# Performance work log

Hardware: AMD Instinct MI355X
Metric: run time of the kernel (lower is better)

Reference implementation:

```python
import jax, jax.numpy as jnp
import numpy as np

H = 2048          # hidden_size
NQ = 16           # num_q_heads
NKV = 4           # num_kv_heads
HD = H // NQ      # head_dim = 128
REP = NQ // NKV   # kv repeat factor
FF = 8192         # intermediate_size
B, S = 2, 2048
EPS = 1e-6


def setup_inputs() -> dict:
    key = jax.random.key(0)
    ks = jax.random.split(key, 12)
    sd = 0.02
    return {
        "hidden_states": jax.random.normal(ks[0], (B, S, H), jnp.float32),
        "Wq": jax.random.normal(ks[1], (H, H), jnp.float32) * sd,
        "bq": jnp.zeros((H,), jnp.float32),
        "Wk": jax.random.normal(ks[2], (H, NKV * HD), jnp.float32) * sd,
        "bk": jnp.zeros((NKV * HD,), jnp.float32),
        "Wv": jax.random.normal(ks[3], (H, NKV * HD), jnp.float32) * sd,
        "bv": jnp.zeros((NKV * HD,), jnp.float32),
        "Wo": jax.random.normal(ks[4], (H, H), jnp.float32) * sd,
        "bo": jnp.zeros((H,), jnp.float32),
        "W1": jax.random.normal(ks[5], (H, FF), jnp.float32) * sd,
        "b1": jnp.zeros((FF,), jnp.float32),
        "W2": jax.random.normal(ks[6], (FF, H), jnp.float32) * sd,
        "b2": jnp.zeros((H,), jnp.float32),
        "g1": jnp.ones((H,), jnp.float32),  # ln1 weight
        "g2": jnp.ones((H,), jnp.float32),  # ln2 weight
    }


def _rmsnorm(x, g):
    rms = jnp.sqrt(jnp.mean(x * x, axis=-1, keepdims=True) + EPS)
    return g * (x / rms)


def _attention(x, Wq, bq, Wk, bk, Wv, bv, Wo, bo):
    b, s, _ = x.shape
    q = (x @ Wq + bq).reshape(b, s, NQ, HD).transpose(0, 2, 1, 3)    # [b,hq,s,d]
    k = (x @ Wk + bk).reshape(b, s, NKV, HD).transpose(0, 2, 1, 3)   # [b,hkv,s,d]
    v = (x @ Wv + bv).reshape(b, s, NKV, HD).transpose(0, 2, 1, 3)
    k = jnp.repeat(k, REP, axis=1)  # GQA: repeat_interleave over head dim
    v = jnp.repeat(v, REP, axis=1)
    scale = 1.0 / np.sqrt(HD).astype(np.float32)
    scores = jnp.einsum("bhqd,bhkd->bhqk", q, k) * scale
    causal = jnp.triu(jnp.ones((s, s), bool), k=1)                   # True above diag
    scores = jnp.where(causal[None, None], -jnp.inf, scores)
    probs = jax.nn.softmax(scores, axis=-1)
    ctx = jnp.einsum("bhqk,bhkd->bhqd", probs, v)
    ctx = ctx.transpose(0, 2, 1, 3).reshape(b, s, H)
    return ctx @ Wo + bo


def reference(hidden_states, Wq, bq, Wk, bk, Wv, bv, Wo, bo, W1, b1, W2, b2, g1, g2):
    x = hidden_states
    # pre-norm attention block
    x = x + _attention(_rmsnorm(x, g1), Wq, bq, Wk, bk, Wv, bv, Wo, bo)
    # pre-norm FFN block (exact GELU, matching torch nn.GELU default)
    h = _rmsnorm(x, g2)
    h = jax.nn.gelu(h @ W1 + b1, approximate=False) @ W2 + b2
    return x + h
```

## Files before the change

### kernel.cpp

```cpp
#include <hip/hip_runtime.h>
#include <cstdint>

#define H_    2048
#define NQ_   16
#define NKV_  4
#define HD_   128
#define FF_   8192
#define B_    2
#define S_    2048
#define TOK   (B_*S_)
#define QKVN  (H_ + 2*NKV_*HD_)
#define KVB   64

typedef __bf16 bf16;
typedef bf16  bf16x8 __attribute__((ext_vector_type(8)));
typedef float f32x4  __attribute__((ext_vector_type(4)));

typedef __attribute__((address_space(1))) void as1_void;
typedef __attribute__((address_space(3))) void as3_void;

__device__ __forceinline__ void gload_lds16(const void* g, void* l) {
    __builtin_amdgcn_global_load_lds((as1_void*)g, (as3_void*)l, 16, 0, 0);
}

__global__ __launch_bounds__(256) void wtrans_kernel(
    const float* __restrict__ W, bf16* __restrict__ Wt, int K, int N, int outOff)
{
    __shared__ float tile[32][33];
    const int n0 = (int)blockIdx.x * 32;
    const int k0 = (int)blockIdx.y * 32;
    const int c  = (int)threadIdx.x & 31;
    const int r  = (int)threadIdx.x >> 5;
#pragma unroll
    for (int i = 0; i < 4; ++i)
        tile[r + i*8][c] = W[(size_t)(k0 + r + i*8) * N + n0 + c];
    __syncthreads();
#pragma unroll
    for (int i = 0; i < 4; ++i)
        Wt[(size_t)(outOff + n0 + r + i*8) * K + k0 + c] = (bf16)tile[c][r + i*8];
}

__global__ void biaspack_kernel(const float* __restrict__ bq, const float* __restrict__ bk,
                                const float* __restrict__ bv, float* __restrict__ out)
{
    const int i = (int)(blockIdx.x * 256 + threadIdx.x);
    out[i] = (i < H_) ? bq[i] : (i < H_ + NKV_*HD_ ? bk[i - H_] : bv[i - H_ - NKV_*HD_]);
}

__global__ __launch_bounds__(256) void rmsnorm_kernel(
    const float* __restrict__ x, const float* __restrict__ g, bf16* __restrict__ y)
{
    const int row = (int)blockIdx.x;
    const int tid = (int)threadIdx.x;
    const float* xr = x + (size_t)row * H_;
    const float4 a = *(const float4*)(xr + tid*8);
    const float4 c = *(const float4*)(xr + tid*8 + 4);
    float ss = a.x*a.x + a.y*a.y + a.z*a.z + a.w*a.w
             + c.x*c.x + c.y*c.y + c.z*c.z + c.w*c.w;
#pragma unroll
    for (int d = 1; d < 64; d <<= 1) ss += __shfl_xor(ss, d);
    __shared__ float red[4];
    if ((tid & 63) == 0) red[tid >> 6] = ss;
    __syncthreads();
    const float inv = rsqrtf((red[0]+red[1]+red[2]+red[3]) * (1.0f/H_) + 1e-6f);
    const float vals[8] = {a.x,a.y,a.z,a.w,c.x,c.y,c.z,c.w};
    const float* gp = g + tid*8;
    bf16x8 outv;
#pragma unroll
    for (int e = 0; e < 8; ++e) outv[e] = (bf16)(vals[e] * inv * gp[e]);
    *(bf16x8*)(y + (size_t)row * H_ + tid*8) = outv;
}

__global__ __launch_bounds__(256) void vtrans_kernel(
    const bf16* __restrict__ qkv, bf16* __restrict__ Vt)
{
    __shared__ bf16 tile[32][33];
    const int tt = (int)blockIdx.x;
    const int d0 = (int)blockIdx.y * 32;
    const int kh = (int)blockIdx.z;
    const int b  = (tt*32) / S_;
    const int s0 = (tt*32) % S_;
    const int c = (int)threadIdx.x & 31;
    const int r = (int)threadIdx.x >> 5;
#pragma unroll
    for (int i = 0; i < 4; ++i)
        tile[r + i*8][c] = qkv[(size_t)(tt*32 + r + i*8)*QKVN + H_ + NKV_*HD_ + kh*HD_ + d0 + c];
    __syncthreads();
#pragma unroll
    for (int i = 0; i < 4; ++i)
        Vt[((size_t)(b*NKV_ + kh)*HD_ + d0 + r + i*8)*S_ + s0 + c] = tile[c][r + i*8];
}

template<int MODE>
__global__ __launch_bounds__(256) void gemm_kernel(
    const bf16* __restrict__ A, const bf16* __restrict__ Bt,
    const float* __restrict__ bias, const float* __restrict__ resid,
    void* __restrict__ Cout, int M, int N, int K)
{
    __shared__ bf16 lA[128*64];
    __shared__ bf16 lB[128*64];
    const int tid  = (int)threadIdx.x;
    const int wid  = tid >> 6;
    const int lane = tid & 63;
    const int lr   = lane & 15;
    const int lg   = lane >> 4;
    const int m0 = (int)blockIdx.y * 128;
    const int n0 = (int)blockIdx.x * 128;
    const int wm = (wid >> 1) * 64;
    const int wn = (wid & 1) * 64;

    f32x4 acc[4][4] = {};

    const int sRow = wid*32 + (lane >> 3);
    const int sCol = ((lane & 7) ^ (lane >> 3)) * 8;
    const bf16* aSrc = A  + (size_t)(m0 + sRow) * K + sCol;
    const bf16* bSrc = Bt + (size_t)(n0 + sRow) * K + sCol;

    for (int k0 = 0; k0 < K; k0 += 64) {
#pragma unroll
        for (int i = 0; i < 4; ++i) {
            gload_lds16(aSrc + (size_t)(i*8)*K + k0, &lA[(wid*32 + i*8)*64]);
            gload_lds16(bSrc + (size_t)(i*8)*K + k0, &lB[(wid*32 + i*8)*64]);
        }
        __syncthreads();
#pragma unroll
        for (int kk = 0; kk < 64; kk += 32) {
            const int ks = (kk + lg*8) ^ ((lr & 7) * 8);
            bf16x8 af[4], bfr[4];
#pragma unroll
            for (int i = 0; i < 4; ++i)
                af[i] = *(const bf16x8*)&lA[(wm + i*16 + lr)*64 + ks];
#pragma unroll
            for (int j = 0; j < 4; ++j)
                bfr[j] = *(const bf16x8*)&lB[(wn + j*16 + lr)*64 + ks];
#pragma unroll
            for (int i = 0; i < 4; ++i)
#pragma unroll
                for (int j = 0; j < 4; ++j)
                    acc[i][j] = __builtin_amdgcn_mfma_f32_16x16x32_bf16(
                        af[i], bfr[j], acc[i][j], 0, 0, 0);
        }
        __syncthreads();
    }

#pragma unroll
    for (int j = 0; j < 4; ++j) {
        const int col = n0 + wn + j*16 + lr;
        const float bj = bias[col];
#pragma unroll
        for (int i = 0; i < 4; ++i) {
            const int row0 = m0 + wm + i*16 + lg*4;
#pragma unroll
            for (int rr = 0; rr < 4; ++rr) {
                float v = acc[i][j][rr] + bj;
                const size_t idx = (size_t)(row0 + rr) * N + col;
                if (MODE == 2) {
                    ((float*)Cout)[idx] = v + resid[idx];
                } else {
                    if (MODE == 1) v = 0.5f * v * (1.0f + erff(v * 0.70710678118654752f));
                    ((bf16*)Cout)[idx] = (bf16)v;
                }
            }
        }
    }
}

__global__ __launch_bounds__(256) void attn_kernel(
    const bf16* __restrict__ qkv, const bf16* __restrict__ Vt,
    bf16* __restrict__ ctx)
{
    __shared__ bf16 lK[2][KVB*HD_];
    __shared__ bf16 lV[2][HD_*KVB];
    __shared__ bf16 lP[4][16*72];
    const int tid  = (int)threadIdx.x;
    const int wid  = tid >> 6;
    const int lane = tid & 63;
    const int lr   = lane & 15;
    const int lg   = lane >> 4;
    const int qt = (int)gridDim.x - 1 - (int)blockIdx.x;
    const int h = (int)blockIdx.y, b = (int)blockIdx.z;
    const int kh = h >> 2;
    const int qb = qt * 64;
    const int qw = qb + wid * 16;
    const float scale = 0.08838834764831845f;

    const bf16* kB[4];
    const bf16* vB[4];
#pragma unroll
    for (int i = 0; i < 4; ++i) {
        const int kRow = (wid*4 + i)*4 + (lane >> 4);
        const int kCol = ((lane & 15) ^ (kRow & 7)) * 8;
        kB[i] = qkv + (size_t)(b*S_ + kRow)*QKVN + H_ + kh*HD_ + kCol;
        const int vRow = (wid*4 + i)*8 + (lane >> 3);
        const int vCol = ((lane & 7) ^ (vRow & 7)) * 8;
        vB[i] = Vt + ((size_t)(b*NKV_ + kh)*HD_ + vRow)*S_ + vCol;
    }

    bf16x8 qf[4];
    {
        const bf16* qp = qkv + (size_t)(b*S_ + qw + lr)*QKVN + h*HD_ + lg*8;
#pragma unroll
        for (int t = 0; t < 4; ++t) qf[t] = *(const bf16x8*)(qp + t*32);
    }

    f32x4 o[8] = {};
    float mrow[4] = {-__builtin_inff(), -__builtin_inff(), -__builtin_inff(), -__builtin_inff()};
    float lrow[4] = {0.f, 0.f, 0.f, 0.f};
    const int nt = qt + 1;

#pragma unroll
    for (int i = 0; i < 4; ++i) {
        gload_lds16(kB[i], &lK[0][(wid*4 + i)*4*HD_]);
        gload_lds16(vB[i], &lV[0][(wid*4 + i)*8*KVB]);
    }

    int cur = 0;
    for (int t = 0; t < nt; ++t) {
        __syncthreads();
        if (t + 1 < nt) {
            const size_t kAdd = (size_t)(t+1)*KVB*QKVN;
            const size_t vAdd = (size_t)(t+1)*KVB;
#pragma unroll
            for (int i = 0; i < 4; ++i) {
                gload_lds16(kB[i] + kAdd, &lK[cur^1][(wid*4 + i)*4*HD_]);
                gload_lds16(vB[i] + vAdd, &lV[cur^1][(wid*4 + i)*8*KVB]);
            }
        }
        const int kv0 = t * KVB;

        f32x4 s[4] = {};
#pragma unroll
        for (int sub = 0; sub < 4; ++sub) {
            const int krow = sub*16 + lr;
            const bf16* kr = &lK[cur][krow*HD_];
            const int sw = (krow & 7) * 8;
#pragma unroll
            for (int d = 0; d < 4; ++d) {
                const bf16x8 kf = *(const bf16x8*)(kr + ((d*32 + lg*8) ^ sw));
                s[sub] = __builtin_amdgcn_mfma_f32_16x16x32_bf16(qf[d], kf, s[sub], 0, 0, 0);
            }
        }

        float p[4][4], rmax[4];
        if (t == qt) {
#pragma unroll
            for (int rr = 0; rr < 4; ++rr) {
                const int q = qw + lg*4 + rr;
                rmax[rr] = -__builtin_inff();
#pragma unroll
                for (int sub = 0; sub < 4; ++sub) {
                    const int kv = kv0 + sub*16 + lr;
                    const float v = s[sub][rr] * scale;
                    p[sub][rr] = (kv <= q) ? v : -__builtin_inff();
                    rmax[rr] = fmaxf(rmax[rr], p[sub][rr]);
                }
            }
        } else {
#pragma unroll
            for (int rr = 0; rr < 4; ++rr) {
                rmax[rr] = -__builtin_inff();
#pragma unroll
                for (int sub = 0; sub < 4; ++sub) {
                    p[sub][rr] = s[sub][rr] * scale;
                    rmax[rr] = fmaxf(rmax[rr], p[sub][rr]);
                }
            }
        }
#pragma unroll
        for (int d = 1; d < 16; d <<= 1)
#pragma unroll
            for (int rr = 0; rr < 4; ++rr)
                rmax[rr] = fmaxf(rmax[rr], __shfl_xor(rmax[rr], d));

        float fsc[4], rsum[4];
#pragma unroll
        for (int rr = 0; rr < 4; ++rr) {
            const float mn = fmaxf(mrow[rr], rmax[rr]);
            fsc[rr]  = __expf(mrow[rr] - mn);
            mrow[rr] = mn;
            rsum[rr] = 0.f;
#pragma unroll
            for (int sub = 0; sub < 4; ++sub) {
                p[sub][rr] = __expf(p[sub][rr] - mn);
                rsum[rr] += p[sub][rr];
            }
        }
#pragma unroll
        for (int d = 1; d < 16; d <<= 1)
#pragma unroll
            for (int rr = 0; rr < 4; ++rr)
                rsum[rr] += __shfl_xor(rsum[rr], d);
#pragma unroll
        for (int rr = 0; rr < 4; ++rr) lrow[rr] = lrow[rr]*fsc[rr] + rsum[rr];
#pragma unroll
        for (int dch = 0; dch < 8; ++dch)
#pragma unroll
            for (int rr = 0; rr < 4; ++rr) o[dch][rr] *= fsc[rr];

#pragma unroll
        for (int sub = 0; sub < 4; ++sub)
#pragma unroll
            for (int rr = 0; rr < 4; ++rr)
                lP[wid][(lg*4 + rr)*72 + sub*16 + lr] = (bf16)p[sub][rr];
        bf16x8 pf[2];
#pragma unroll
        for (int kk = 0; kk < 2; ++kk)
            pf[kk] = *(const bf16x8*)&lP[wid][lr*72 + kk*32 + lg*8];

#pragma unroll
        for (int dch = 0; dch < 8; ++dch) {
            const bf16* vr = &lV[cur][(dch*16 + lr)*KVB];
            const int sw = (lr & 7) * 8;
#pragma unroll
            for (int kk = 0; kk < 2; ++kk) {
                const bf16x8 vf = *(const bf16x8*)(vr + ((kk*32 + lg*8) ^ sw));
                o[dch] = __builtin_amdgcn_mfma_f32_16x16x32_bf16(pf[kk], vf, o[dch], 0, 0, 0);
            }
        }
        cur ^= 1;
    }

#pragma unroll
    for (int rr = 0; rr < 4; ++rr) {
        const float inv = 1.0f / lrow[rr];
        bf16* cp = ctx + (size_t)(b*S_ + qw + lg*4 + rr) * H_ + h*HD_ + lr;
#pragma unroll
        for (int dch = 0; dch < 8; ++dch)
            cp[dch*16] = (bf16)(o[dch][rr] * inv);
    }
}

extern "C" void kernel_launch(void* const* d_in, const int* in_sizes, int n_in,
                              void* d_out, int out_size, void* d_ws, size_t ws_size,
                              hipStream_t stream)
{
    const float* hidden = (const float*)d_in[0];
    const float* Wq = (const float*)d_in[1];
    const float* bq = (const float*)d_in[2];
    const float* Wk = (const float*)d_in[3];
    const float* bk = (const float*)d_in[4];
    const float* Wv = (const float*)d_in[5];
    const float* bv = (const float*)d_in[6];
    const float* Wo = (const float*)d_in[7];
    const float* bo = (const float*)d_in[8];
    const float* W1 = (const float*)d_in[9];
    const float* b1 = (const float*)d_in[10];
    const float* W2 = (const float*)d_in[11];
    const float* b2 = (const float*)d_in[12];
    const float* g1 = (const float*)d_in[13];
    const float* g2 = (const float*)d_in[14];
    float* out = (float*)d_out;

    char* p = (char*)d_ws;
    auto alloc = [&](size_t bytes) { char* r = p; p += (bytes + 255) & ~(size_t)255; return r; };
    bf16*  wt_qkv = (bf16*)alloc((size_t)QKVN * H_ * 2);
    bf16*  wo_t   = (bf16*)alloc((size_t)H_ * H_ * 2);
    bf16*  w1_t   = (bf16*)alloc((size_t)FF_ * H_ * 2);
    bf16*  w2_t   = (bf16*)alloc((size_t)H_ * FF_ * 2);
    float* bqkv   = (float*)alloc((size_t)QKVN * 4);
    bf16*  xn1    = (bf16*)alloc((size_t)TOK * H_ * 2);
    bf16*  qkv    = (bf16*)alloc((size_t)TOK * QKVN * 2);
    bf16*  ctxb   = (bf16*)alloc((size_t)TOK * H_ * 2);
    float* x1     = (float*)alloc((size_t)TOK * H_ * 4);
    bf16*  xn2    = (bf16*)alloc((size_t)TOK * H_ * 2);
    bf16*  ffn    = (bf16*)alloc((size_t)TOK * FF_ * 2);
    bf16*  vt     = xn1;

    const dim3 blk(256);
    biaspack_kernel<<<dim3(QKVN/256), blk, 0, stream>>>(bq, bk, bv, bqkv);
    wtrans_kernel<<<dim3(H_/32,  H_/32),  blk, 0, stream>>>(Wq, wt_qkv, H_, H_,  0);
    wtrans_kernel<<<dim3(512/32, H_/32),  blk, 0, stream>>>(Wk, wt_qkv, H_, 512, H_);
    wtrans_kernel<<<dim3(512/32, H_/32),  blk, 0, stream>>>(Wv, wt_qkv, H_, 512, H_ + 512);
    wtrans_kernel<<<dim3(H_/32,  H_/32),  blk, 0, stream>>>(Wo, wo_t,   H_, H_,  0);
    wtrans_kernel<<<dim3(FF_/32, H_/32),  blk, 0, stream>>>(W1, w1_t,   H_, FF_, 0);
    wtrans_kernel<<<dim3(H_/32,  FF_/32), blk, 0, stream>>>(W2, w2_t,   FF_, H_, 0);

    rmsnorm_kernel<<<dim3(TOK), blk, 0, stream>>>(hidden, g1, xn1);
    gemm_kernel<0><<<dim3(QKVN/128, TOK/128), blk, 0, stream>>>(
        xn1, wt_qkv, bqkv, nullptr, qkv, TOK, QKVN, H_);
    vtrans_kernel<<<dim3(TOK/32, HD_/32, NKV_), blk, 0, stream>>>(qkv, vt);
    attn_kernel<<<dim3(S_/64, NQ_, B_), blk, 0, stream>>>(qkv, vt, ctxb);
    gemm_kernel<2><<<dim3(H_/128, TOK/128), blk, 0, stream>>>(
        ctxb, wo_t, bo, hidden, x1, TOK, H_, H_);
    rmsnorm_kernel<<<dim3(TOK), blk, 0, stream>>>(x1, g2, xn2);
    gemm_kernel<1><<<dim3(FF_/128, TOK/128), blk, 0, stream>>>(
        xn2, w1_t, b1, nullptr, ffn, TOK, FF_, H_);
    gemm_kernel<2><<<dim3(H_/128, TOK/128), blk, 0, stream>>>(
        ffn, w2_t, b2, x1, out, TOK, H_, FF_);
}
```

Measured before the change: 758.1 us.

## Replace GEMM with 256x128 triple-buffered 8-wave pipelined kernel

The old 128x128 single-buffered GEMM is replaced by a 512-thread kernel with 256x128 tiles and a three-stage LDS ring. Global-to-LDS prefetch of tile t+2 is interleaved with MFMA work in two half-phases, and s_setprio, sched_barrier and explicit waitcnts are used to overlap memory with compute. It also remaps workgroup IDs in an XCD-aware order to improve L2 locality, and uses a different LDS swizzle. The aim is to hide load latency and raise MFMA utilisation in the GEMMs that dominate runtime. The cost is more LDS per block, one block per CU, and fragile hand-managed vmcnt accounting.

Result: no change. 753.1 us (-0.7%).

```diff
diff --git a/kernel.cpp b/kernel.cpp
--- a/kernel.cpp
+++ b/kernel.cpp
@@ -12,6 +12,10 @@
 #define QKVN  (H_ + 2*NKV_*HD_)
 #define KVB   64
 
+#define BM 256
+#define BN 128
+#define BKG 64
+
 typedef __bf16 bf16;
 typedef bf16  bf16x8 __attribute__((ext_vector_type(8)));
 typedef float f32x4  __attribute__((ext_vector_type(4)));
@@ -92,67 +96,136 @@
 }
 
 template<int MODE>
-__global__ __launch_bounds__(256) void gemm_kernel(
+__global__ __launch_bounds__(512, 1) void gemm2_kernel(
     const bf16* __restrict__ A, const bf16* __restrict__ Bt,
     const float* __restrict__ bias, const float* __restrict__ resid,
     void* __restrict__ Cout, int M, int N, int K)
 {
-    __shared__ bf16 lA[128*64];
-    __shared__ bf16 lB[128*64];
+    __shared__ bf16 lA[3][BM*BKG];
+    __shared__ bf16 lB[3][BN*BKG];
     const int tid  = (int)threadIdx.x;
     const int wid  = tid >> 6;
     const int lane = tid & 63;
     const int lr   = lane & 15;
     const int lg   = lane >> 4;
-    const int m0 = (int)blockIdx.y * 128;
-    const int n0 = (int)blockIdx.x * 128;
-    const int wm = (wid >> 1) * 64;
-    const int wn = (wid & 1) * 64;
+
+    const int gx  = (int)gridDim.x;
+    const int nwg = gx * (int)gridDim.y;
+    int wg = (int)blockIdx.y * gx + (int)blockIdx.x;
+    if ((nwg & 7) == 0) wg = (wg & 7) * (nwg >> 3) + (wg >> 3);
+    const int n0 = (wg % gx) * BN;
+    const int m0 = (wg / gx) * BM;
+
+    const int wr = wid >> 1;
+    const int wc = wid & 1;
+
+    const int srow = wid*8 + (lane >> 3);
+    const int scol = ((lane & 7) * 8) ^ ((wid & 1) * 16);
+    const bf16* aS = A  + (size_t)(m0 + srow) * K + scol;
+    const bf16* bS = Bt + (size_t)(n0 + srow) * K + scol;
 
     f32x4 acc[4][4] = {};
-
-    const int sRow = wid*32 + (lane >> 3);
-    const int sCol = ((lane & 7) ^ (lane >> 3)) * 8;
-    const bf16* aSrc = A  + (size_t)(m0 + sRow) * K + sCol;
-    const bf16* bSrc = Bt + (size_t)(n0 + sRow) * K + sCol;
-
-    for (int k0 = 0; k0 < K; k0 += 64) {
-#pragma unroll
-        for (int i = 0; i < 4; ++i) {
-            gload_lds16(aSrc + (size_t)(i*8)*K + k0, &lA[(wid*32 + i*8)*64]);
-            gload_lds16(bSrc + (size_t)(i*8)*K + k0, &lB[(wid*32 + i*8)*64]);
-        }
-        __syncthreads();
-#pragma unroll
-        for (int kk = 0; kk < 64; kk += 32) {
-            const int ks = (kk + lg*8) ^ ((lr & 7) * 8);
-            bf16x8 af[4], bfr[4];
-#pragma unroll
-            for (int i = 0; i < 4; ++i)
-                af[i] = *(const bf16x8*)&lA[(wm + i*16 + lr)*64 + ks];
-#pragma unroll
-            for (int j = 0; j < 4; ++j)
-                bfr[j] = *(const bf16x8*)&lB[(wn + j*16 + lr)*64 + ks];
-#pragma unroll
-            for (int i = 0; i < 4; ++i)
-#pragma unroll
-                for (int j = 0; j < 4; ++j)
-                    acc[i][j] = __builtin_amdgcn_mfma_f32_16x16x32_bf16(
-                        af[i], bfr[j], acc[i][j], 0, 0, 0);
-        }
-        __syncthreads();
-    }
-
-#pragma unroll
-    for (int j = 0; j < 4; ++j) {
-        const int col = n0 + wn + j*16 + lr;
+    const int nt = K / BKG;
+
+#pragma unroll
+    for (int i = 0; i < 4; ++i)
+        gload_lds16(aS + (size_t)i*64*K, &lA[0][(i*64 + wid*8)*BKG]);
+#pragma unroll
+    for (int j = 0; j < 2; ++j)
+        gload_lds16(bS + (size_t)j*64*K, &lB[0][(j*64 + wid*8)*BKG]);
+#pragma unroll
+    for (int i = 0; i < 4; ++i)
+        gload_lds16(aS + (size_t)i*64*K + BKG, &lA[1][(i*64 + wid*8)*BKG]);
+#pragma unroll
+    for (int j = 0; j < 2; ++j)
+        gload_lds16(bS + (size_t)j*64*K + BKG, &lB[1][(j*64 + wid*8)*BKG]);
+    asm volatile("s_waitcnt vmcnt(6)" ::: "memory");
+    __builtin_amdgcn_s_barrier();
+
+    const int sw = ((lane >> 3) & 1) * 16;
+    int cur = 0;
+    for (int t = 0; t < nt; ++t) {
+        const bf16* lAc = lA[cur];
+        const bf16* lBc = lB[cur];
+        const int   pc  = (cur + 2 >= 3) ? cur - 1 : cur + 2;
+        const size_t nk0 = (size_t)(t + 2) * BKG;
+        const bool  pf  = (t + 2) < nt;
+
+        bf16x8 af[2][2], bfr[4][2];
+#pragma unroll
+        for (int mf = 0; mf < 2; ++mf)
+#pragma unroll
+            for (int ks = 0; ks < 2; ++ks)
+                af[mf][ks] = *(const bf16x8*)&lAc[(wr*64 + mf*16 + lr)*BKG + ((ks*32 + lg*8) ^ sw)];
+#pragma unroll
+        for (int nf = 0; nf < 4; ++nf)
+#pragma unroll
+            for (int ks = 0; ks < 2; ++ks)
+                bfr[nf][ks] = *(const bf16x8*)&lBc[(wc*64 + nf*16 + lr)*BKG + ((ks*32 + lg*8) ^ sw)];
+        if (pf) {
+            gload_lds16(aS + (size_t)0*64*K + nk0, &lA[pc][(0*64 + wid*8)*BKG]);
+            gload_lds16(aS + (size_t)1*64*K + nk0, &lA[pc][(1*64 + wid*8)*BKG]);
+            gload_lds16(aS + (size_t)2*64*K + nk0, &lA[pc][(2*64 + wid*8)*BKG]);
+        }
+        __builtin_amdgcn_s_barrier();
+        asm volatile("s_waitcnt lgkmcnt(0)" ::: "memory");
+        __builtin_amdgcn_sched_barrier(0);
+        __builtin_amdgcn_s_setprio(1);
+#pragma unroll
+        for (int ks = 0; ks < 2; ++ks)
+#pragma unroll
+            for (int mf = 0; mf < 2; ++mf)
+#pragma unroll
+                for (int nf = 0; nf < 4; ++nf)
+                    acc[mf][nf] = __builtin_amdgcn_mfma_f32_16x16x32_bf16(
+                        af[mf][ks], bfr[nf][ks], acc[mf][nf], 0, 0, 0);
+        __builtin_amdgcn_s_setprio(0);
+        __builtin_amdgcn_sched_barrier(0);
+        __builtin_amdgcn_s_barrier();
+
+        bf16x8 af2[2][2];
+#pragma unroll
+        for (int mf = 0; mf < 2; ++mf)
+#pragma unroll
+            for (int ks = 0; ks < 2; ++ks)
+                af2[mf][ks] = *(const bf16x8*)&lAc[(wr*64 + (mf+2)*16 + lr)*BKG + ((ks*32 + lg*8) ^ sw)];
+        if (pf) {
+            gload_lds16(aS + (size_t)3*64*K + nk0, &lA[pc][(3*64 + wid*8)*BKG]);
+            gload_lds16(bS + (size_t)0*64*K + nk0, &lB[pc][(0*64 + wid*8)*BKG]);
+            gload_lds16(bS + (size_t)1*64*K + nk0, &lB[pc][(1*64 + wid*8)*BKG]);
+            asm volatile("s_waitcnt vmcnt(6)" ::: "memory");
+        } else {
+            asm volatile("s_waitcnt vmcnt(0)" ::: "memory");
+        }
+        __builtin_amdgcn_s_barrier();
+        asm volatile("s_waitcnt lgkmcnt(0)" ::: "memory");
+        __builtin_amdgcn_sched_barrier(0);
+        __builtin_amdgcn_s_setprio(1);
+#pragma unroll
+        for (int ks = 0; ks < 2; ++ks)
+#pragma unroll
+            for (int mf = 0; mf < 2; ++mf)
+#pragma unroll
+                for (int nf = 0; nf < 4; ++nf)
+                    acc[mf+2][nf] = __builtin_amdgcn_mfma_f32_16x16x32_bf16(
+                        af2[mf][ks], bfr[nf][ks], acc[mf+2][nf], 0, 0, 0);
+        __builtin_amdgcn_s_setprio(0);
+        __builtin_amdgcn_sched_barrier(0);
+        __builtin_amdgcn_s_barrier();
+
+        cur = (cur + 1 >= 3) ? 0 : cur + 1;
+    }
+
+#pragma unroll
+    for (int nf = 0; nf < 4; ++nf) {
+        const int col = n0 + wc*64 + nf*16 + lr;
         const float bj = bias[col];
 #pragma unroll
-        for (int i = 0; i < 4; ++i) {
-            const int row0 = m0 + wm + i*16 + lg*4;
+        for (int mf = 0; mf < 4; ++mf) {
+            const int row0 = m0 + wr*64 + mf*16 + lg*4;
 #pragma unroll
             for (int rr = 0; rr < 4; ++rr) {
-                float v = acc[i][j][rr] + bj;
+                float v = acc[mf][nf][rr] + bj;
                 const size_t idx = (size_t)(row0 + rr) * N + col;
                 if (MODE == 2) {
                     ((float*)Cout)[idx] = v + resid[idx];
@@ -233,10 +306,10 @@
         for (int sub = 0; sub < 4; ++sub) {
             const int krow = sub*16 + lr;
             const bf16* kr = &lK[cur][krow*HD_];
-            const int sw = (krow & 7) * 8;
+            const int swk = (krow & 7) * 8;
 #pragma unroll
             for (int d = 0; d < 4; ++d) {
-                const bf16x8 kf = *(const bf16x8*)(kr + ((d*32 + lg*8) ^ sw));
+                const bf16x8 kf = *(const bf16x8*)(kr + ((d*32 + lg*8) ^ swk));
                 s[sub] = __builtin_amdgcn_mfma_f32_16x16x32_bf16(qf[d], kf, s[sub], 0, 0, 0);
             }
         }
@@ -302,19 +375,19 @@
 #pragma unroll
             for (int rr = 0; rr < 4; ++rr)
                 lP[wid][(lg*4 + rr)*72 + sub*16 + lr] = (bf16)p[sub][rr];
-        bf16x8 pf[2];
+        bf16x8 pfr[2];
 #pragma unroll
         for (int kk = 0; kk < 2; ++kk)
-            pf[kk] = *(const bf16x8*)&lP[wid][lr*72 + kk*32 + lg*8];
+            pfr[kk] = *(const bf16x8*)&lP[wid][lr*72 + kk*32 + lg*8];
 
 #pragma unroll
         for (int dch = 0; dch < 8; ++dch) {
             const bf16* vr = &lV[cur][(dch*16 + lr)*KVB];
-            const int sw = (lr & 7) * 8;
+            const int swv = (lr & 7) * 8;
 #pragma unroll
             for (int kk = 0; kk < 2; ++kk) {
-                const bf16x8 vf = *(const bf16x8*)(vr + ((kk*32 + lg*8) ^ sw));
-                o[dch] = __builtin_amdgcn_mfma_f32_16x16x32_bf16(pf[kk], vf, o[dch], 0, 0, 0);
+                const bf16x8 vf = *(const bf16x8*)(vr + ((kk*32 + lg*8) ^ swv));
+                o[dch] = __builtin_amdgcn_mfma_f32_16x16x32_bf16(pfr[kk], vf, o[dch], 0, 0, 0);
             }
         }
         cur ^= 1;
@@ -367,6 +440,7 @@
     bf16*  vt     = xn1;
 
     const dim3 blk(256);
+    const dim3 blk2(512);
     biaspack_kernel<<<dim3(QKVN/256), blk, 0, stream>>>(bq, bk, bv, bqkv);
     wtrans_kernel<<<dim3(H_/32,  H_/32),  blk, 0, stream>>>(Wq, wt_qkv, H_, H_,  0);
     wtrans_kernel<<<dim3(512/32, H_/32),  blk, 0, stream>>>(Wk, wt_qkv, H_, 512, H_);
@@ -376,15 +450,15 @@
     wtrans_kernel<<<dim3(H_/32,  FF_/32), blk, 0, stream>>>(W2, w2_t,   FF_, H_, 0);
 
     rmsnorm_kernel<<<dim3(TOK), blk, 0, stream>>>(hidden, g1, xn1);
-    gemm_kernel<0><<<dim3(QKVN/128, TOK/128), blk, 0, stream>>>(
+    gemm2_kernel<0><<<dim3(QKVN/BN, TOK/BM), blk2, 0, stream>>>(
         xn1, wt_qkv, bqkv, nullptr, qkv, TOK, QKVN, H_);
     vtrans_kernel<<<dim3(TOK/32, HD_/32, NKV_), blk, 0, stream>>>(qkv, vt);
     attn_kernel<<<dim3(S_/64, NQ_, B_), blk, 0, stream>>>(qkv, vt, ctxb);
-    gemm_kernel<2><<<dim3(H_/128, TOK/128), blk, 0, stream>>>(
+    gemm2_kernel<2><<<dim3(H_/BN, TOK/BM), blk2, 0, stream>>>(
         ctxb, wo_t, bo, hidden, x1, TOK, H_, H_);
     rmsnorm_kernel<<<dim3(TOK), blk, 0, stream>>>(x1, g2, xn2);
-    gemm_kernel<1><<<dim3(FF_/128, TOK/128), blk, 0, stream>>>(
+    gemm2_kernel<1><<<dim3(FF_/BN, TOK/BM), blk2, 0, stream>>>(
         xn2, w1_t, b1, nullptr, ffn, TOK, FF_, H_);
-    gemm_kernel<2><<<dim3(H_/128, TOK/128), blk, 0, stream>>>(
+    gemm2_kernel<2><<<dim3(H_/BN, TOK/BM), blk2, 0, stream>>>(
         ffn, w2_t, b2, x1, out, TOK, H_, FF_);
 }
```

## Replace GEMM with 256x256 double-buffered 8-wave kernel and split-K W2 GEMM

Applied to the files above, without the earlier changes.

Swaps the 128x128 single-buffered GEMM for a 256x256 tile kernel with 512 threads. It double-buffers LDS through async global-to-LDS loads and interleaves MFMA clusters with staged loads under explicit waitcnt and barriers. Workgroup IDs are remapped for locality, and setprio is raised during MFMA bursts. The FFN down-projection (K=8192) now uses split-K over two partitions that write bf16 partials into the freed W1 buffer, followed by a reduce kernel that adds bias and residual. The aim is higher MFMA utilisation and better tile reuse. The cost is bf16 rounding of the partial sums, an extra reduce pass, and heavy LDS use (128KB per block).

New measurement: 757.4 us. Within noise of the previous version (-0.1%).

```diff
diff --git a/kernel.cpp b/kernel.cpp
--- a/kernel.cpp
+++ b/kernel.cpp
@@ -92,70 +92,177 @@
 }
 
 template<int MODE>
-__global__ __launch_bounds__(256) void gemm_kernel(
+__global__ __launch_bounds__(512, 2) void gemm3_kernel(
     const bf16* __restrict__ A, const bf16* __restrict__ Bt,
     const float* __restrict__ bias, const float* __restrict__ resid,
-    void* __restrict__ Cout, int M, int N, int K)
-{
-    __shared__ bf16 lA[128*64];
-    __shared__ bf16 lB[128*64];
+    void* __restrict__ Cout, int M, int N, int Kf, int Ks)
+{
+    __shared__ bf16 lA[2][256*64];
+    __shared__ bf16 lB[2][256*64];
     const int tid  = (int)threadIdx.x;
     const int wid  = tid >> 6;
     const int lane = tid & 63;
     const int lr   = lane & 15;
     const int lg   = lane >> 4;
-    const int m0 = (int)blockIdx.y * 128;
-    const int n0 = (int)blockIdx.x * 128;
-    const int wm = (wid >> 1) * 64;
-    const int wn = (wid & 1) * 64;
-
-    f32x4 acc[4][4] = {};
-
-    const int sRow = wid*32 + (lane >> 3);
-    const int sCol = ((lane & 7) ^ (lane >> 3)) * 8;
-    const bf16* aSrc = A  + (size_t)(m0 + sRow) * K + sCol;
-    const bf16* bSrc = Bt + (size_t)(n0 + sRow) * K + sCol;
-
-    for (int k0 = 0; k0 < K; k0 += 64) {
-#pragma unroll
-        for (int i = 0; i < 4; ++i) {
-            gload_lds16(aSrc + (size_t)(i*8)*K + k0, &lA[(wid*32 + i*8)*64]);
-            gload_lds16(bSrc + (size_t)(i*8)*K + k0, &lB[(wid*32 + i*8)*64]);
-        }
-        __syncthreads();
-#pragma unroll
-        for (int kk = 0; kk < 64; kk += 32) {
-            const int ks = (kk + lg*8) ^ ((lr & 7) * 8);
-            bf16x8 af[4], bfr[4];
-#pragma unroll
-            for (int i = 0; i < 4; ++i)
-                af[i] = *(const bf16x8*)&lA[(wm + i*16 + lr)*64 + ks];
-#pragma unroll
-            for (int j = 0; j < 4; ++j)
-                bfr[j] = *(const bf16x8*)&lB[(wn + j*16 + lr)*64 + ks];
-#pragma unroll
-            for (int i = 0; i < 4; ++i)
-#pragma unroll
-                for (int j = 0; j < 4; ++j)
-                    acc[i][j] = __builtin_amdgcn_mfma_f32_16x16x32_bf16(
-                        af[i], bfr[j], acc[i][j], 0, 0, 0);
-        }
-        __syncthreads();
-    }
-
-#pragma unroll
-    for (int j = 0; j < 4; ++j) {
-        const int col = n0 + wn + j*16 + lr;
-        const float bj = bias[col];
-#pragma unroll
-        for (int i = 0; i < 4; ++i) {
-            const int row0 = m0 + wm + i*16 + lg*4;
+    const int z    = (int)blockIdx.z;
+    const int kOff = z * Ks;
+
+    const int gx  = (int)gridDim.x;
+    const int nwg = gx * (int)gridDim.y;
+    int wg = (int)blockIdx.y * gx + (int)blockIdx.x;
+    wg = (wg & 7) * (nwg >> 3) + (wg >> 3);
+    const int n0 = (wg % gx) * 256;
+    const int m0 = (wg / gx) * 256;
+
+    const int wm = wid >> 2;
+    const int wn = wid & 3;
+
+    const int r8     = lane >> 3;
+    const int srcOct = (lane & 7) ^ (((lane >> 5) & 1) << 1);
+    const bf16* aB0 = A  + (size_t)(m0 + wid*16 + r8) * Kf + kOff + srcOct*8;
+    const bf16* aB1 = aB0 + (size_t)8 * Kf;
+    const bf16* bB0 = Bt + (size_t)(n0 + wid*16 + r8) * Kf + kOff + srcOct*8;
+    const bf16* bB1 = bB0 + (size_t)8 * Kf;
+
+    const int NT = Ks / 64;
+    const int NITER = NT / 2;
+
+    auto stA = [&](int k, int half, int buf) {
+        const size_t ka = (size_t)k * 64;
+        gload_lds16(aB0 + (size_t)half*128*Kf + ka, &lA[buf][(half*128 + wid*16    )*64]);
+        gload_lds16(aB1 + (size_t)half*128*Kf + ka, &lA[buf][(half*128 + wid*16 + 8)*64]);
+    };
+    auto stB = [&](int k, int half, int buf) {
+        const size_t ka = (size_t)k * 64;
+        gload_lds16(bB0 + (size_t)half*128*Kf + ka, &lB[buf][(half*128 + wid*16    )*64]);
+        gload_lds16(bB1 + (size_t)half*128*Kf + ka, &lB[buf][(half*128 + wid*16 + 8)*64]);
+    };
+    auto rd = [&](const bf16* base, int row, int kk) -> bf16x8 {
+        return *(const bf16x8*)&base[row*64 + ((kk*32 + lg*8) ^ (((row >> 2) & 1) << 4))];
+    };
+
+    f32x4 acc[8][4] = {};
+    bf16x8 fa[4][2], fb0[2][2], fb1[2][2];
+
+    stA(0,0,0); stB(0,0,0); stB(0,1,0); stA(0,1,0);
+    stA(1,0,1); stB(1,0,1); stB(1,1,1);
+    asm volatile("s_waitcnt vmcnt(6)" ::: "memory");
+    __builtin_amdgcn_s_barrier();
+
+#define MFMA_CLUSTER(ACCR, FB)                                              \
+    __builtin_amdgcn_s_setprio(1);                                          \
+    _Pragma("unroll") for (int kk = 0; kk < 2; ++kk)                        \
+    _Pragma("unroll") for (int mf = 0; mf < 4; ++mf)                        \
+    _Pragma("unroll") for (int nf = 0; nf < 2; ++nf)                        \
+        acc[ACCR][(FB) ? nf+2 : nf] = __builtin_amdgcn_mfma_f32_16x16x32_bf16( \
+            fa[mf][kk], ((FB) ? fb1 : fb0)[nf][kk], acc[ACCR][(FB) ? nf+2 : nf], 0, 0, 0); \
+    __builtin_amdgcn_s_setprio(0);                                          \
+    __builtin_amdgcn_sched_barrier(0);
+
+    for (int t = 0; t < NITER; ++t) {
+        const int kb0 = 2*t, kb1 = 2*t + 1;
+        const bool s2 = (kb0 + 2) < NT;
+        const bool s3 = (kb1 + 2) < NT;
+        const bool lastGate = (t == NITER - 1);
+
+#pragma unroll
+        for (int mf = 0; mf < 4; ++mf) { fa[mf][0] = rd(lA[0], wm*64 + mf*16 + lr, 0);
+                                         fa[mf][1] = rd(lA[0], wm*64 + mf*16 + lr, 1); }
+#pragma unroll
+        for (int nf = 0; nf < 2; ++nf) { fb0[nf][0] = rd(lB[0], wn*64 + nf*16 + lr, 0);
+                                         fb0[nf][1] = rd(lB[0], wn*64 + nf*16 + lr, 1); }
+        stA(kb1, 1, 1);
+        __builtin_amdgcn_s_barrier();
+        asm volatile("s_waitcnt lgkmcnt(0)" ::: "memory");
+        __builtin_amdgcn_sched_barrier(0);
+        MFMA_CLUSTER(mf, 0)
+        __builtin_amdgcn_s_barrier();
+
+#pragma unroll
+        for (int nf = 0; nf < 2; ++nf) { fb1[nf][0] = rd(lB[0], wn*64 + 32 + nf*16 + lr, 0);
+                                         fb1[nf][1] = rd(lB[0], wn*64 + 32 + nf*16 + lr, 1); }
+        if (s2) stA(kb0 + 2, 0, 0);
+        __builtin_amdgcn_s_barrier();
+        asm volatile("s_waitcnt lgkmcnt(0)" ::: "memory");
+        __builtin_amdgcn_sched_barrier(0);
+        MFMA_CLUSTER(mf, 1)
+        __builtin_amdgcn_s_barrier();
+
+#pragma unroll
+        for (int mf = 0; mf < 4; ++mf) { fa[mf][0] = rd(lA[0], 128 + wm*64 + mf*16 + lr, 0);
+                                         fa[mf][1] = rd(lA[0], 128 + wm*64 + mf*16 + lr, 1); }
+        if (s2) stB(kb0 + 2, 0, 0);
+        __builtin_amdgcn_s_barrier();
+        asm volatile("s_waitcnt lgkmcnt(0)" ::: "memory");
+        __builtin_amdgcn_sched_barrier(0);
+        MFMA_CLUSTER(mf+4, 1)
+        __builtin_amdgcn_s_barrier();
+
+        if (s2) stB(kb0 + 2, 1, 0);
+        __builtin_amdgcn_s_barrier();
+        __builtin_amdgcn_sched_barrier(0);
+        MFMA_CLUSTER(mf+4, 0)
+        if (lastGate) { asm volatile("s_waitcnt vmcnt(0)" ::: "memory"); }
+        else          { asm volatile("s_waitcnt vmcnt(6)" ::: "memory"); }
+        __builtin_amdgcn_s_barrier();
+
+#pragma unroll
+        for (int mf = 0; mf < 4; ++mf) { fa[mf][0] = rd(lA[1], wm*64 + mf*16 + lr, 0);
+                                         fa[mf][1] = rd(lA[1], wm*64 + mf*16 + lr, 1); }
+#pragma unroll
+        for (int nf = 0; nf < 2; ++nf) { fb0[nf][0] = rd(lB[1], wn*64 + nf*16 + lr, 0);
+                                         fb0[nf][1] = rd(lB[1], wn*64 + nf*16 + lr, 1); }
+        if (s2) stA(kb0 + 2, 1, 0);
+        __builtin_amdgcn_s_barrier();
+        asm volatile("s_waitcnt lgkmcnt(0)" ::: "memory");
+        __builtin_amdgcn_sched_barrier(0);
+        MFMA_CLUSTER(mf, 0)
+        __builtin_amdgcn_s_barrier();
+
+#pragma unroll
+        for (int nf = 0; nf < 2; ++nf) { fb1[nf][0] = rd(lB[1], wn*64 + 32 + nf*16 + lr, 0);
+                                         fb1[nf][1] = rd(lB[1], wn*64 + 32 + nf*16 + lr, 1); }
+        if (s3) stA(kb1 + 2, 0, 1);
+        __builtin_amdgcn_s_barrier();
+        asm volatile("s_waitcnt lgkmcnt(0)" ::: "memory");
+        __builtin_amdgcn_sched_barrier(0);
+        MFMA_CLUSTER(mf, 1)
+        __builtin_amdgcn_s_barrier();
+
+#pragma unroll
+        for (int mf = 0; mf < 4; ++mf) { fa[mf][0] = rd(lA[1], 128 + wm*64 + mf*16 + lr, 0);
+                                         fa[mf][1] = rd(lA[1], 128 + wm*64 + mf*16 + lr, 1); }
+        if (s3) stB(kb1 + 2, 0, 1);
+        __builtin_amdgcn_s_barrier();
+        asm volatile("s_waitcnt lgkmcnt(0)" ::: "memory");
+        __builtin_amdgcn_sched_barrier(0);
+        MFMA_CLUSTER(mf+4, 1)
+        __builtin_amdgcn_s_barrier();
+
+        if (s3) stB(kb1 + 2, 1, 1);
+        __builtin_amdgcn_s_barrier();
+        __builtin_amdgcn_sched_barrier(0);
+        MFMA_CLUSTER(mf+4, 0)
+        if (!lastGate) { asm volatile("s_waitcnt vmcnt(6)" ::: "memory"); }
+        __builtin_amdgcn_s_barrier();
+    }
+#undef MFMA_CLUSTER
+
+#pragma unroll
+    for (int nf = 0; nf < 4; ++nf) {
+        const int col = n0 + wn*64 + nf*16 + lr;
+        const float bj = (MODE == 3) ? 0.f : bias[col];
+#pragma unroll
+        for (int mf = 0; mf < 8; ++mf) {
+            const int row0 = m0 + (mf >> 2)*128 + wm*64 + (mf & 3)*16 + lg*4;
 #pragma unroll
             for (int rr = 0; rr < 4; ++rr) {
-                float v = acc[i][j][rr] + bj;
+                float v = acc[mf][nf][rr] + bj;
                 const size_t idx = (size_t)(row0 + rr) * N + col;
                 if (MODE == 2) {
                     ((float*)Cout)[idx] = v + resid[idx];
+                } else if (MODE == 3) {
+                    ((bf16*)Cout)[(size_t)z * M * N + idx] = (bf16)v;
                 } else {
                     if (MODE == 1) v = 0.5f * v * (1.0f + erff(v * 0.70710678118654752f));
                     ((bf16*)Cout)[idx] = (bf16)v;
@@ -163,6 +270,31 @@
             }
         }
     }
+}
+
+__global__ __launch_bounds__(256) void reduce2_kernel(
+    const bf16* __restrict__ part, const float* __restrict__ bias,
+    const float* __restrict__ resid, float* __restrict__ out)
+{
+    const size_t i0 = ((size_t)blockIdx.x * 256 + threadIdx.x) * 8;
+    const bf16x8 p0 = *(const bf16x8*)(part + i0);
+    const bf16x8 p1 = *(const bf16x8*)(part + (size_t)TOK*H_ + i0);
+    const int col = (int)(i0 & (H_ - 1));
+    const float4 r0 = *(const float4*)(resid + i0);
+    const float4 r1 = *(const float4*)(resid + i0 + 4);
+    const float4 b0 = *(const float4*)(bias + col);
+    const float4 b1 = *(const float4*)(bias + col + 4);
+    float4 o0, o1;
+    o0.x = (float)p0[0] + (float)p1[0] + b0.x + r0.x;
+    o0.y = (float)p0[1] + (float)p1[1] + b0.y + r0.y;
+    o0.z = (float)p0[2] + (float)p1[2] + b0.z + r0.z;
+    o0.w = (float)p0[3] + (float)p1[3] + b0.w + r0.w;
+    o1.x = (float)p0[4] + (float)p1[4] + b1.x + r1.x;
+    o1.y = (float)p0[5] + (float)p1[5] + b1.y + r1.y;
+    o1.z = (float)p0[6] + (float)p1[6] + b1.z + r1.z;
+    o1.w = (float)p0[7] + (float)p1[7] + b1.w + r1.w;
+    *(float4*)(out + i0)     = o0;
+    *(float4*)(out + i0 + 4) = o1;
 }
 
 __global__ __launch_bounds__(256) void attn_kernel(
@@ -233,10 +365,10 @@
         for (int sub = 0; sub < 4; ++sub) {
             const int krow = sub*16 + lr;
             const bf16* kr = &lK[cur][krow*HD_];
-            const int sw = (krow & 7) * 8;
+            const int swk = (krow & 7) * 8;
 #pragma unroll
             for (int d = 0; d < 4; ++d) {
-                const bf16x8 kf = *(const bf16x8*)(kr + ((d*32 + lg*8) ^ sw));
+                const bf16x8 kf = *(const bf16x8*)(kr + ((d*32 + lg*8) ^ swk));
                 s[sub] = __builtin_amdgcn_mfma_f32_16x16x32_bf16(qf[d], kf, s[sub], 0, 0, 0);
             }
         }
@@ -302,19 +434,19 @@
 #pragma unroll
             for (int rr = 0; rr < 4; ++rr)
                 lP[wid][(lg*4 + rr)*72 + sub*16 + lr] = (bf16)p[sub][rr];
-        bf16x8 pf[2];
+        bf16x8 pfr[2];
 #pragma unroll
         for (int kk = 0; kk < 2; ++kk)
-            pf[kk] = *(const bf16x8*)&lP[wid][lr*72 + kk*32 + lg*8];
+            pfr[kk] = *(const bf16x8*)&lP[wid][lr*72 + kk*32 + lg*8];
 
 #pragma unroll
         for (int dch = 0; dch < 8; ++dch) {
             const bf16* vr = &lV[cur][(dch*16 + lr)*KVB];
-            const int sw = (lr & 7) * 8;
+            const int swv = (lr & 7) * 8;
 #pragma unroll
             for (int kk = 0; kk < 2; ++kk) {
-                const bf16x8 vf = *(const bf16x8*)(vr + ((kk*32 + lg*8) ^ sw));
-                o[dch] = __builtin_amdgcn_mfma_f32_16x16x32_bf16(pf[kk], vf, o[dch], 0, 0, 0);
+                const bf16x8 vf = *(const bf16x8*)(vr + ((kk*32 + lg*8) ^ swv));
+                o[dch] = __builtin_amdgcn_mfma_f32_16x16x32_bf16(pfr[kk], vf, o[dch], 0, 0, 0);
             }
         }
         cur ^= 1;
@@ -365,8 +497,10 @@
     bf16*  xn2    = (bf16*)alloc((size_t)TOK * H_ * 2);
     bf16*  ffn    = (bf16*)alloc((size_t)TOK * FF_ * 2);
     bf16*  vt     = xn1;
+    bf16*  fpart  = w1_t;
 
     const dim3 blk(256);
+    const dim3 blk3(512);
     biaspack_kernel<<<dim3(QKVN/256), blk, 0, stream>>>(bq, bk, bv, bqkv);
     wtrans_kernel<<<dim3(H_/32,  H_/32),  blk, 0, stream>>>(Wq, wt_qkv, H_, H_,  0);
     wtrans_kernel<<<dim3(512/32, H_/32),  blk, 0, stream>>>(Wk, wt_qkv, H_, 512, H_);
@@ -376,15 +510,16 @@
     wtrans_kernel<<<dim3(H_/32,  FF_/32), blk, 0, stream>>>(W2, w2_t,   FF_, H_, 0);
 
     rmsnorm_kernel<<<dim3(TOK), blk, 0, stream>>>(hidden, g1, xn1);
-    gemm_kernel<0><<<dim3(QKVN/128, TOK/128), blk, 0, stream>>>(
-        xn1, wt_qkv, bqkv, nullptr, qkv, TOK, QKVN, H_);
+    gemm3_kernel<0><<<dim3(QKVN/256, TOK/256), blk3, 0, stream>>>(
+        xn1, wt_qkv, bqkv, nullptr, qkv, TOK, QKVN, H_, H_);
     vtrans_kernel<<<dim3(TOK/32, HD_/32, NKV_), blk, 0, stream>>>(qkv, vt);
     attn_kernel<<<dim3(S_/64, NQ_, B_), blk, 0, stream>>>(qkv, vt, ctxb);
-    gemm_kernel<2><<<dim3(H_/128, TOK/128), blk, 0, stream>>>(
-        ctxb, wo_t, bo, hidden, x1, TOK, H_, H_);
+    gemm3_kernel<2><<<dim3(H_/256, TOK/256), blk3, 0, stream>>>(
+        ctxb, wo_t, bo, hidden, x1, TOK, H_, H_, H_);
     rmsnorm_kernel<<<dim3(TOK), blk, 0, stream>>>(x1, g2, xn2);
-    gemm_kernel<1><<<dim3(FF_/128, TOK/128), blk, 0, stream>>>(
-        xn2, w1_t, b1, nullptr, ffn, TOK, FF_, H_);
-    gemm_kernel<2><<<dim3(H_/128, TOK/128), blk, 0, stream>>>(
-        ffn, w2_t, b2, x1, out, TOK, H_, FF_);
-}
+    gemm3_kernel<1><<<dim3(FF_/256, TOK/256), blk3, 0, stream>>>(
+        xn2, w1_t, b1, nullptr, ffn, TOK, FF_, H_, H_);
+    gemm3_kernel<3><<<dim3(H_/256, TOK/256, 2), blk3, 0, stream>>>(
+        ffn, w2_t, nullptr, nullptr, fpart, TOK, H_, FF_, FF_/2);
+    reduce2_kernel<<<dim3(TOK*H_/(256*8)), blk, 0, stream>>>(fpart, b2, x1, out);
+}
```

## Switch GEMMs to 32x32 MFMA with grouped tile order and split-K FFN down-projection

Applied to the files above, without the earlier changes.

Replaces the GEMM kernel's 16x16x32 MFMA tiling with 32x32x16 MFMA fragments and a new LDS swizzle. It also remaps workgroup IDs into grouped supertiles for better L2 reuse across the XCDs. The W2 GEMM is split along K into two halves: partials go to bf16 buffers in the freed w1_t workspace, then a new reduce kernel adds bias and residual. The split-K raises parallelism for the long-K down-projection but adds a reduction pass and rounds the partial sums to bf16.

New measurement: 810.9 us. 1.07x slower.

```diff
diff --git a/kernel.cpp b/kernel.cpp
--- a/kernel.cpp
+++ b/kernel.cpp
@@ -15,6 +15,7 @@
 typedef __bf16 bf16;
 typedef bf16  bf16x8 __attribute__((ext_vector_type(8)));
 typedef float f32x4  __attribute__((ext_vector_type(4)));
+typedef float f32x16 __attribute__((ext_vector_type(16)));
 
 typedef __attribute__((address_space(1))) void as1_void;
 typedef __attribute__((address_space(3))) void as3_void;
@@ -92,70 +93,88 @@
 }
 
 template<int MODE>
-__global__ __launch_bounds__(256) void gemm_kernel(
+__global__ __launch_bounds__(256) void gemm5_kernel(
     const bf16* __restrict__ A, const bf16* __restrict__ Bt,
     const float* __restrict__ bias, const float* __restrict__ resid,
-    void* __restrict__ Cout, int M, int N, int K)
+    void* __restrict__ Cout, int M, int N, int Kf, int Ks)
 {
     __shared__ bf16 lA[128*64];
     __shared__ bf16 lB[128*64];
     const int tid  = (int)threadIdx.x;
     const int wid  = tid >> 6;
     const int lane = tid & 63;
-    const int lr   = lane & 15;
-    const int lg   = lane >> 4;
-    const int m0 = (int)blockIdx.y * 128;
-    const int n0 = (int)blockIdx.x * 128;
+    const int l31  = lane & 31;
+    const int hi   = lane >> 5;
+    const int z    = (int)blockIdx.z;
+    const int kOff = z * Ks;
+
+    const int gx  = (int)gridDim.x;
+    const int nwg = gx * (int)gridDim.y;
+    int wg = (int)blockIdx.y * gx + (int)blockIdx.x;
+    wg = (wg & 7) * (nwg >> 3) + (wg >> 3);
+    const int nsup  = gx >> 2;
+    const int chunk = wg >> 5;
+    const int cin   = wg & 31;
+    const int m0 = ((chunk / nsup) * 8 + (cin >> 2)) * 128;
+    const int n0 = ((chunk % nsup) * 4 + (cin & 3)) * 128;
+
     const int wm = (wid >> 1) * 64;
     const int wn = (wid & 1) * 64;
 
-    f32x4 acc[4][4] = {};
-
-    const int sRow = wid*32 + (lane >> 3);
-    const int sCol = ((lane & 7) ^ (lane >> 3)) * 8;
-    const bf16* aSrc = A  + (size_t)(m0 + sRow) * K + sCol;
-    const bf16* bSrc = Bt + (size_t)(n0 + sRow) * K + sCol;
-
-    for (int k0 = 0; k0 < K; k0 += 64) {
+    const int r8   = lane >> 3;
+    const int octS = (lane & 7) ^ (((lane >> 3) & 3) << 1);
+    const bf16* aS = A  + (size_t)(m0 + wid*32 + r8) * Kf + kOff + octS*8;
+    const bf16* bS = Bt + (size_t)(n0 + wid*32 + r8) * Kf + kOff + octS*8;
+
+    const int NT = Ks / 64;
+
+    auto rdf = [&](const bf16* base, int row, int kk) -> bf16x8 {
+        return *(const bf16x8*)&base[row*64 + ((kk*16 + hi*8) ^ ((row & 3) << 4))];
+    };
+
+    f32x16 acc[2][2] = {};
+
+    for (int kt = 0; kt < NT; ++kt) {
+        const size_t ka = (size_t)kt * 64;
 #pragma unroll
         for (int i = 0; i < 4; ++i) {
-            gload_lds16(aSrc + (size_t)(i*8)*K + k0, &lA[(wid*32 + i*8)*64]);
-            gload_lds16(bSrc + (size_t)(i*8)*K + k0, &lB[(wid*32 + i*8)*64]);
+            gload_lds16(aS + (size_t)(i*8)*Kf + ka, &lA[(wid*32 + i*8)*64]);
+            gload_lds16(bS + (size_t)(i*8)*Kf + ka, &lB[(wid*32 + i*8)*64]);
         }
         __syncthreads();
 #pragma unroll
-        for (int kk = 0; kk < 64; kk += 32) {
-            const int ks = (kk + lg*8) ^ ((lr & 7) * 8);
-            bf16x8 af[4], bfr[4];
-#pragma unroll
-            for (int i = 0; i < 4; ++i)
-                af[i] = *(const bf16x8*)&lA[(wm + i*16 + lr)*64 + ks];
-#pragma unroll
-            for (int j = 0; j < 4; ++j)
-                bfr[j] = *(const bf16x8*)&lB[(wn + j*16 + lr)*64 + ks];
-#pragma unroll
-            for (int i = 0; i < 4; ++i)
-#pragma unroll
-                for (int j = 0; j < 4; ++j)
-                    acc[i][j] = __builtin_amdgcn_mfma_f32_16x16x32_bf16(
-                        af[i], bfr[j], acc[i][j], 0, 0, 0);
+        for (int kk = 0; kk < 4; ++kk) {
+            bf16x8 af[2], bfr[2];
+#pragma unroll
+            for (int mf = 0; mf < 2; ++mf) af[mf]  = rdf(lA, wm + mf*32 + l31, kk);
+#pragma unroll
+            for (int nf = 0; nf < 2; ++nf) bfr[nf] = rdf(lB, wn + nf*32 + l31, kk);
+#pragma unroll
+            for (int mf = 0; mf < 2; ++mf)
+#pragma unroll
+                for (int nf = 0; nf < 2; ++nf)
+                    acc[mf][nf] = __builtin_amdgcn_mfma_f32_32x32x16_bf16(
+                        af[mf], bfr[nf], acc[mf][nf], 0, 0, 0);
         }
         __syncthreads();
     }
 
 #pragma unroll
-    for (int j = 0; j < 4; ++j) {
-        const int col = n0 + wn + j*16 + lr;
-        const float bj = bias[col];
-#pragma unroll
-        for (int i = 0; i < 4; ++i) {
-            const int row0 = m0 + wm + i*16 + lg*4;
-#pragma unroll
-            for (int rr = 0; rr < 4; ++rr) {
-                float v = acc[i][j][rr] + bj;
-                const size_t idx = (size_t)(row0 + rr) * N + col;
+    for (int nf = 0; nf < 2; ++nf) {
+        const int col = n0 + wn + nf*32 + l31;
+        const float bj = (MODE == 3) ? 0.f : bias[col];
+#pragma unroll
+        for (int mf = 0; mf < 2; ++mf) {
+            const int rbase = m0 + wm + mf*32 + 4*hi;
+#pragma unroll
+            for (int reg = 0; reg < 16; ++reg) {
+                const int row = rbase + (reg & 3) + 8*(reg >> 2);
+                float v = acc[mf][nf][reg] + bj;
+                const size_t idx = (size_t)row * N + col;
                 if (MODE == 2) {
                     ((float*)Cout)[idx] = v + resid[idx];
+                } else if (MODE == 3) {
+                    ((bf16*)Cout)[(size_t)z * M * N + idx] = (bf16)v;
                 } else {
                     if (MODE == 1) v = 0.5f * v * (1.0f + erff(v * 0.70710678118654752f));
                     ((bf16*)Cout)[idx] = (bf16)v;
@@ -163,6 +182,31 @@
             }
         }
     }
+}
+
+__global__ __launch_bounds__(256) void reduce2_kernel(
+    const bf16* __restrict__ part, const float* __restrict__ bias,
+    const float* __restrict__ resid, float* __restrict__ out)
+{
+    const size_t i0 = ((size_t)blockIdx.x * 256 + threadIdx.x) * 8;
+    const bf16x8 p0 = *(const bf16x8*)(part + i0);
+    const bf16x8 p1 = *(const bf16x8*)(part + (size_t)TOK*H_ + i0);
+    const int col = (int)(i0 & (H_ - 1));
+    const float4 r0 = *(const float4*)(resid + i0);
+    const float4 r1 = *(const float4*)(resid + i0 + 4);
+    const float4 b0 = *(const float4*)(bias + col);
+    const float4 b1 = *(const float4*)(bias + col + 4);
+    float4 o0, o1;
+    o0.x = (float)p0[0] + (float)p1[0] + b0.x + r0.x;
+    o0.y = (float)p0[1] + (float)p1[1] + b0.y + r0.y;
+    o0.z = (float)p0[2] + (float)p1[2] + b0.z + r0.z;
+    o0.w = (float)p0[3] + (float)p1[3] + b0.w + r0.w;
+    o1.x = (float)p0[4] + (float)p1[4] + b1.x + r1.x;
+    o1.y = (float)p0[5] + (float)p1[5] + b1.y + r1.y;
+    o1.z = (float)p0[6] + (float)p1[6] + b1.z + r1.z;
+    o1.w = (float)p0[7] + (float)p1[7] + b1.w + r1.w;
+    *(float4*)(out + i0)     = o0;
+    *(float4*)(out + i0 + 4) = o1;
 }
 
 __global__ __launch_bounds__(256) void attn_kernel(
@@ -233,10 +277,10 @@
         for (int sub = 0; sub < 4; ++sub) {
             const int krow = sub*16 + lr;
             const bf16* kr = &lK[cur][krow*HD_];
-            const int sw = (krow & 7) * 8;
+            const int swk = (krow & 7) * 8;
 #pragma unroll
             for (int d = 0; d < 4; ++d) {
-                const bf16x8 kf = *(const bf16x8*)(kr + ((d*32 + lg*8) ^ sw));
+                const bf16x8 kf = *(const bf16x8*)(kr + ((d*32 + lg*8) ^ swk));
                 s[sub] = __builtin_amdgcn_mfma_f32_16x16x32_bf16(qf[d], kf, s[sub], 0, 0, 0);
             }
         }
@@ -302,19 +346,19 @@
 #pragma unroll
             for (int rr = 0; rr < 4; ++rr)
                 lP[wid][(lg*4 + rr)*72 + sub*16 + lr] = (bf16)p[sub][rr];
-        bf16x8 pf[2];
+        bf16x8 pfr[2];
 #pragma unroll
         for (int kk = 0; kk < 2; ++kk)
-            pf[kk] = *(const bf16x8*)&lP[wid][lr*72 + kk*32 + lg*8];
+            pfr[kk] = *(const bf16x8*)&lP[wid][lr*72 + kk*32 + lg*8];
 
 #pragma unroll
         for (int dch = 0; dch < 8; ++dch) {
             const bf16* vr = &lV[cur][(dch*16 + lr)*KVB];
-            const int sw = (lr & 7) * 8;
+            const int swv = (lr & 7) * 8;
 #pragma unroll
             for (int kk = 0; kk < 2; ++kk) {
-                const bf16x8 vf = *(const bf16x8*)(vr + ((kk*32 + lg*8) ^ sw));
-                o[dch] = __builtin_amdgcn_mfma_f32_16x16x32_bf16(pf[kk], vf, o[dch], 0, 0, 0);
+                const bf16x8 vf = *(const bf16x8*)(vr + ((kk*32 + lg*8) ^ swv));
+                o[dch] = __builtin_amdgcn_mfma_f32_16x16x32_bf16(pfr[kk], vf, o[dch], 0, 0, 0);
             }
         }
         cur ^= 1;
@@ -365,6 +409,7 @@
     bf16*  xn2    = (bf16*)alloc((size_t)TOK * H_ * 2);
     bf16*  ffn    = (bf16*)alloc((size_t)TOK * FF_ * 2);
     bf16*  vt     = xn1;
+    bf16*  fpart  = w1_t;
 
     const dim3 blk(256);
     biaspack_kernel<<<dim3(QKVN/256), blk, 0, stream>>>(bq, bk, bv, bqkv);
@@ -376,15 +421,16 @@
     wtrans_kernel<<<dim3(H_/32,  FF_/32), blk, 0, stream>>>(W2, w2_t,   FF_, H_, 0);
 
     rmsnorm_kernel<<<dim3(TOK), blk, 0, stream>>>(hidden, g1, xn1);
-    gemm_kernel<0><<<dim3(QKVN/128, TOK/128), blk, 0, stream>>>(
-        xn1, wt_qkv, bqkv, nullptr, qkv, TOK, QKVN, H_);
+    gemm5_kernel<0><<<dim3(QKVN/128, TOK/128), blk, 0, stream>>>(
+        xn1, wt_qkv, bqkv, nullptr, qkv, TOK, QKVN, H_, H_);
     vtrans_kernel<<<dim3(TOK/32, HD_/32, NKV_), blk, 0, stream>>>(qkv, vt);
     attn_kernel<<<dim3(S_/64, NQ_, B_), blk, 0, stream>>>(qkv, vt, ctxb);
-    gemm_kernel<2><<<dim3(H_/128, TOK/128), blk, 0, stream>>>(
-        ctxb, wo_t, bo, hidden, x1, TOK, H_, H_);
+    gemm5_kernel<2><<<dim3(H_/128, TOK/128), blk, 0, stream>>>(
+        ctxb, wo_t, bo, hidden, x1, TOK, H_, H_, H_);
     rmsnorm_kernel<<<dim3(TOK), blk, 0, stream>>>(x1, g2, xn2);
-    gemm_kernel<1><<<dim3(FF_/128, TOK/128), blk, 0, stream>>>(
-        xn2, w1_t, b1, nullptr, ffn, TOK, FF_, H_);
-    gemm_kernel<2><<<dim3(H_/128, TOK/128), blk, 0, stream>>>(
-        ffn, w2_t, b2, x1, out, TOK, H_, FF_);
-}
+    gemm5_kernel<1><<<dim3(FF_/128, TOK/128), blk, 0, stream>>>(
+        xn2, w1_t, b1, nullptr, ffn, TOK, FF_, H_, H_);
+    gemm5_kernel<3><<<dim3(H_/128, TOK/128, 2), blk, 0, stream>>>(
+        ffn, w2_t, nullptr, nullptr, fpart, TOK, H_, FF_, FF_/2);
+    reduce2_kernel<<<dim3(TOK*H_/(256*8)), blk, 0, stream>>>(fpart, b2, x1, out);
+}
```
